# Kernel optimization log

Hardware: AMD Instinct MI355X
Metric: run time of the kernel (lower is better)

The kernel has to match this reference:

```python
import jax, jax.numpy as jnp
import numpy as np

HID = 64      # LSTM hidden size
UH_LEN = 15   # unit-hydrograph length (days)
N_INC = 4     # SAC-SMA sub-steps per day

# (name, lo, hi) -> sigmoid-scaled physical parameter ranges
PARAM_SPECS = [
    ("HAMON_COEF", 0.5, 2.0),
    ("SCF", 0.7, 1.4), ("PXTEMP", -2.0, 2.0), ("MFMAX", 0.5, 2.0), ("MFMIN", 0.05, 0.49),
    ("UADJ", 0.03, 0.19), ("MBASE", 0.0, 1.0), ("TIPM", 0.1, 1.0), ("PLWHC", 0.02, 0.3),
    ("NMF", 0.05, 0.5), ("DAYGM", 0.0, 0.3),
    ("UZTWM", 10.0, 300.0), ("UZFWM", 5.0, 150.0), ("LZTWM", 10.0, 500.0), ("LZFPM", 10.0, 1000.0),
    ("LZFSM", 5.0, 400.0), ("UZK", 0.1, 0.75), ("LZPK", 0.001, 0.05), ("LZSK", 0.01, 0.35),
    ("ZPERC", 5.0, 350.0), ("REXP", 1.0, 5.0), ("PFREE", 0.0, 0.8), ("PCTIM", 0.0, 0.1),
    ("ADIMP", 0.0, 0.4), ("RIVA", 0.0, 0.2), ("SIDE", 0.0, 0.5), ("RSERV", 0.0, 0.4),
    ("THETA_C", 0.0, 1.0), ("UH_N", 1.0, 6.0), ("UH_TAU", 0.5, 5.0),
]


def parameter_net(x_dyn, x_static, Wih, Whh, b_lstm, Ws, bs, Wout, bout):
    """gA: LSTM over dynamic inputs + static encoder -> per-unit physical params."""
    N = x_dyn.shape[0]
    h0 = jnp.zeros((N, HID), x_dyn.dtype)

    def step(carry, xt):
        h, c = carry
        z = xt @ Wih.T + h @ Whh.T + b_lstm
        i, f, g, o = jnp.split(z, 4, axis=-1)
        c = jax.nn.sigmoid(f) * c + jax.nn.sigmoid(i) * jnp.tanh(g)
        h = jax.nn.sigmoid(o) * jnp.tanh(c)
        return (h, c), None

    (h, _), _ = jax.lax.scan(step, (h0, h0), jnp.swapaxes(x_dyn, 0, 1))
    s = jnp.tanh(x_static @ Ws.T + bs)
    raw = jnp.concatenate([h, s], axis=-1) @ Wout.T + bout  # (N, n_params)
    g = jax.nn.sigmoid(raw)
    return {name: lo + g[:, k] * (hi - lo) for k, (name, lo, hi) in enumerate(PARAM_SPECS)}


def hamon_pet(tavg, doyf, lat_rad, coef):
    decl = 0.4093 * jnp.sin(2.0 * jnp.pi / 365.0 * doyf - 1.405)
    cosw = jnp.clip(-jnp.tan(lat_rad[:, None]) * jnp.tan(decl), -0.9999, 0.9999)
    daylen = jnp.arccos(cosw) * 24.0 / jnp.pi                   # hours
    esat = 0.6108 * jnp.exp(17.27 * tavg / (tavg + 237.3))      # kPa
    pet = coef[:, None] * 29.8 * daylen * esat / (tavg + 273.2)
    return jnp.maximum(pet, 0.0)


def run_snow17(prcp, tavg, doyf, elev_m, p):
    SCF, PXTEMP, MFMAX, MFMIN = p['SCF'], p['PXTEMP'], p['MFMAX'], p['MFMIN']
    UADJ, MBASE, TIPM, PLWHC = p['UADJ'], p['MBASE'], p['TIPM'], p['PLWHC']
    NMF, DAYGM = p['NMF'], p['DAYGM']
    pa_fac = jnp.exp(-elev_m / 8434.0)  # atmospheric pressure ratio with elevation

    def step(carry, inp):
        wi, wq, ati = carry
        pr, ta, dy = inp
        is_snow = ta <= PXTEMP
        ps = jnp.where(is_snow, pr * SCF, 0.0)
        prain = jnp.where(is_snow, 0.0, pr)
        wi = wi + ps
        mf = 0.5 * (MFMAX + MFMIN) + 0.5 * (MFMAX - MFMIN) * jnp.sin(2.0 * jnp.pi * dy / 366.0)
        ati = ati + TIPM * (jnp.minimum(ta, 0.0) - ati)
        mros = UADJ * pa_fac * jnp.maximum(ta, 0.0) * jnp.where((~is_snow) & (wi > 0.0), prain, 0.0) * 0.0125
        melt = jnp.clip(mf * jnp.maximum(ta - MBASE, 0.0) + mros - NMF * jnp.maximum(-ati, 0.0), 0.0, wi)
        wi = wi - melt
        gm = jnp.minimum(DAYGM, wi)
        wi = wi - gm
        rain_on_pack = jnp.where(wi > 0.0, prain, 0.0)
        rain_free = prain - rain_on_pack
        wq = wq + melt + rain_on_pack
        out = jnp.maximum(wq - PLWHC * wi, 0.0)
        wq = wq - out
        return (wi, wq, ati), out + gm + rain_free

    z = jnp.zeros_like(p['SCF'])
    _, eff = jax.lax.scan(step, (z, z, z), (prcp.T, tavg.T, doyf.T))
    return eff.T  # (N, T)


def run_sacsma(pav, ep, p, n_inc):
    UZTWM, UZFWM, LZTWM = p['UZTWM'], p['UZFWM'], p['LZTWM']
    LZFPM, LZFSM, UZK = p['LZFPM'], p['LZFSM'], p['UZK']
    LZPK, LZSK, ZPERC, REXP = p['LZPK'], p['LZSK'], p['ZPERC'], p['REXP']
    PFREE, PCTIM, ADIMP, SIDE = p['PFREE'], p['PCTIM'], p['ADIMP'], p['SIDE']
    dt = 1.0 / n_inc
    percm = LZFPM * LZPK + LZFSM * LZSK
    lz_max = LZTWM + LZFPM + LZFSM

    def step(carry, inp):
        uztwc, uzfwc, lztwc, lzfpc, lzfsc, adimc = carry
        pr, e = inp
        # evapotranspiration
        e1 = jnp.minimum(e * uztwc / UZTWM, uztwc); uztwc = uztwc - e1
        red = e - e1
        e2 = jnp.minimum(red, uzfwc); uzfwc = uzfwc - e2; red = red - e2
        e3 = jnp.minimum(red * lztwc / (UZTWM + LZTWM), lztwc); lztwc = lztwc - e3
        # impervious + additional impervious area
        roimp = pr * PCTIM
        padimp = pr * ADIMP
        adimc = adimc + padimp
        adsur = padimp * jnp.clip(adimc / (UZTWM + LZTWM), 0.0, 1.0) ** 2
        adimc = jnp.minimum(adimc - adsur, UZTWM + LZTWM)
        surf = roimp + adsur
        base = jnp.zeros_like(pr)
        pinc = pr * (1.0 - PCTIM - ADIMP) * dt
        for _ in range(n_inc):  # unrolled sub-steps (n_inc is small, static)
            bfp = lzfpc * LZPK * dt; bfs = lzfsc * LZSK * dt
            lzfpc = lzfpc - bfp; lzfsc = lzfsc - bfs
            base = base + (bfp + bfs) / (1.0 + SIDE)
            qif = uzfwc * UZK * dt; uzfwc = uzfwc - qif; surf = surf + qif
            lz_def = (LZTWM - lztwc) + (LZFPM - lzfpc) + (LZFSM - lzfsc)
            defr = jnp.clip(lz_def / lz_max, 1e-6, 1.0)
            perc = percm * (1.0 + ZPERC * defr ** REXP) * dt * uzfwc / UZFWM
            perc = jnp.minimum(jnp.minimum(perc, uzfwc), jnp.maximum(lz_def, 0.0))
            uzfwc = uzfwc - perc
            pfree = perc * PFREE
            lztwc = lztwc + perc - pfree
            ex = jnp.maximum(lztwc - LZTWM, 0.0); lztwc = lztwc - ex; pfree = pfree + ex
            dp = jnp.maximum(LZFPM - lzfpc, 0.0); ds = jnp.maximum(LZFSM - lzfsc, 0.0)
            fr = dp / jnp.maximum(dp + ds, 1e-6)
            lzfpc = lzfpc + pfree * fr; lzfsc = lzfsc + pfree * (1.0 - fr)
            exp_ = jnp.maximum(lzfpc - LZFPM, 0.0); lzfpc = lzfpc - exp_; lzfsc = lzfsc + exp_
            exs = jnp.maximum(lzfsc - LZFSM, 0.0); lzfsc = lzfsc - exs; surf = surf + exs
            uztwc = uztwc + pinc
            exu = jnp.maximum(uztwc - UZTWM, 0.0); uztwc = uztwc - exu
            uzfwc = uzfwc + exu
            exf = jnp.maximum(uzfwc - UZFWM, 0.0); uzfwc = uzfwc - exf
            surf = surf + exf
        return (uztwc, uzfwc, lztwc, lzfpc, lzfsc, adimc), (surf, base)

    init = (0.5 * UZTWM, 0.5 * UZFWM, 0.5 * LZTWM, 0.5 * LZFPM, 0.5 * LZFSM, 0.5 * (UZTWM + LZTWM))
    _, (surf, base) = jax.lax.scan(step, init, (pav.T, ep.T))
    return surf.T, base.T  # (N, T)


def route_lohmann(surf, base, uh_n, uh_tau):
    """Gamma-shaped unit hydrograph per unit; causal convolution over time."""
    t = jnp.arange(1.0, UH_LEN + 1.0)  # (L,)
    w = t[None, :] ** (uh_n[:, None] - 1.0) * jnp.exp(-t[None, :] / uh_tau[:, None])
    uh = w / jnp.sum(w, axis=1, keepdims=True)  # (N, L)
    T = surf.shape[1]
    pad = jnp.pad(surf, ((0, 0), (UH_LEN - 1, 0)))
    q = sum(uh[:, l:l + 1] * pad[:, UH_LEN - 1 - l: UH_LEN - 1 - l + T] for l in range(UH_LEN))
    return q + base


def setup_inputs() -> dict:
    key = jax.random.key(0)
    ks = jax.random.split(key, 13)
    N, T, D_DYN, D_STAT, B = 4000, 730, 8, 16, 200
    NP = len(PARAM_SPECS)
    return {
        'x_dyn': jax.random.normal(ks[0], (N, T, D_DYN), jnp.float32),
        'x_static': jax.random.normal(ks[1], (N, D_STAT), jnp.float32),
        'prcp': 10.0 * jax.random.uniform(ks[2], (N, T), jnp.float32),
        'tavg': 5.0 + 8.0 * jax.random.normal(ks[3], (N, T), jnp.float32),
        'doy': jax.random.randint(ks[4], (N, T), 1, 367, jnp.int32),
        'elev_m': 2500.0 * jax.random.uniform(ks[5], (N,), jnp.float32),
        'lat_rad': 0.2 + 0.6 * jax.random.uniform(ks[6], (N,), jnp.float32),
        'area_weight': jax.random.uniform(ks[7], (N,), jnp.float32),
        'basin_index': jax.random.randint(ks[8], (N,), 0, B, jnp.int32),
        'n_basins': B,
        'Wih': 0.1 * jax.random.normal(ks[9], (4 * HID, D_DYN), jnp.float32),
        'Whh': 0.1 * jax.random.normal(ks[10], (4 * HID, HID), jnp.float32),
        'b_lstm': jnp.zeros((4 * HID,), jnp.float32),
        'Ws': 0.1 * jax.random.normal(ks[11], (HID, D_STAT), jnp.float32),
        'bs': jnp.zeros((HID,), jnp.float32),
        'Wout': 0.1 * jax.random.normal(ks[12], (NP, 2 * HID), jnp.float32),
        'bout': jnp.zeros((NP,), jnp.float32),
    }


def reference(x_dyn, x_static, prcp, tavg, doy, elev_m, lat_rad, area_weight,
              basin_index, n_basins, Wih, Whh, b_lstm, Ws, bs, Wout, bout):
    params = parameter_net(x_dyn, x_static, Wih, Whh, b_lstm, Ws, bs, Wout, bout)
    doyf = doy.astype(jnp.float32)
    pet = hamon_pet(tavg, doyf, lat_rad, params['HAMON_COEF'])
    effective_p = run_snow17(prcp, tavg, doyf, elev_m, params)
    surf, base = run_sacsma(effective_p, pet, params, N_INC)
    q_unit = route_lohmann(surf, base, params['UH_N'], params['UH_TAU'])
    w = area_weight[:, None]
    B = int(n_basins)
    q_gauge = jax.ops.segment_sum(q_unit * w, basin_index, num_segments=B)
    q_base_gauge = jax.ops.segment_sum(base * w, basin_index, num_segments=B)
    return q_gauge, q_base_gauge, q_unit
```

## Files before the change

### kernel.cpp

```cpp
#include <hip/hip_runtime.h>
#include <math.h>

#define HID 64
#define UH_LEN 15
#define N_INC 4

#define TWO_PI_365 0.0172142063f
#define TWO_PI_366 0.0171671554f
#define H24_PI     7.63943727f

typedef short short8 __attribute__((ext_vector_type(8)));
typedef float f32x4  __attribute__((ext_vector_type(4)));

__device__ __forceinline__ float frcp(float x){ return __builtin_amdgcn_rcpf(x); }
__device__ __forceinline__ float sigf(float x){ return frcp(1.0f + __expf(-x)); }
__device__ __forceinline__ float tanhfast(float x){ return 1.0f - 2.0f*frcp(__expf(2.0f*x)+1.0f); }

__device__ __forceinline__ unsigned short f2bf(float f){
    unsigned int u = __float_as_uint(f);
    u += 0x7FFF + ((u >> 16) & 1);
    return (unsigned short)(u >> 16);
}
__device__ __forceinline__ float bf2f(unsigned short h){
    return __uint_as_float(((unsigned int)h) << 16);
}

__device__ const float PLO[30] = {0.5f,0.7f,-2.0f,0.5f,0.05f,0.03f,0.0f,0.1f,0.02f,0.05f,0.0f,
                                  10.0f,5.0f,10.0f,10.0f,5.0f,0.1f,0.001f,0.01f,5.0f,1.0f,0.0f,
                                  0.0f,0.0f,0.0f,0.0f,0.0f,0.0f,1.0f,0.5f};
__device__ const float PHI[30] = {2.0f,1.4f,2.0f,2.0f,0.49f,0.19f,1.0f,1.0f,0.3f,0.5f,0.3f,
                                  300.0f,150.0f,500.0f,1000.0f,400.0f,0.75f,0.05f,0.35f,350.0f,5.0f,0.8f,
                                  0.1f,0.4f,0.2f,0.5f,0.4f,1.0f,6.0f,5.0f};
__device__ const float LOGT[15] = {0.0f,0.69314718f,1.09861229f,1.38629436f,1.60943791f,
                                   1.79175947f,1.94591015f,2.07944154f,2.19722458f,2.30258509f,
                                   2.39789527f,2.48490665f,2.56494936f,2.63905733f,2.70805020f};

__global__ void zero_kernel(float* __restrict__ p, int cnt){
    int i = blockIdx.x*256 + threadIdx.x;
    if (i < cnt) p[i] = 0.0f;
}

__global__ __launch_bounds__(256) void xpack_kernel(
    const float* __restrict__ x_dyn, unsigned short* __restrict__ xb, size_t NT)
{
    size_t i = (size_t)blockIdx.x*256 + threadIdx.x;
    if (i >= NT) return;
    const float4 a = ((const float4*)x_dyn)[2*i];
    const float4 b = ((const float4*)x_dyn)[2*i + 1];
    short8 o;
    o[0]=(short)f2bf(a.x); o[1]=(short)f2bf(a.y); o[2]=(short)f2bf(a.z); o[3]=(short)f2bf(a.w);
    o[4]=(short)f2bf(b.x); o[5]=(short)f2bf(b.y); o[6]=(short)f2bf(b.z); o[7]=(short)f2bf(b.w);
    ((short8*)xb)[i] = o;
}

template<bool XB>
__global__ __launch_bounds__(256, 2) void lstm_kernel(
    const float* __restrict__ x_dyn, const unsigned short* __restrict__ xb,
    const float* __restrict__ x_static,
    const float* __restrict__ Wih, const float* __restrict__ Whh,
    const float* __restrict__ b_lstm, const float* __restrict__ Ws,
    const float* __restrict__ bs, const float* __restrict__ Wout,
    const float* __restrict__ bout, float* __restrict__ params,
    int N, int T, int DSTAT)
{
    __shared__ unsigned short h_lds[2][16*64];
    __shared__ float s_sh[16*64];

    const int tid = threadIdx.x;
    const int wv  = tid >> 6;
    const int ln  = tid & 63;
    const int q   = ln >> 4;
    const int r16 = ln & 15;
    const int u0  = blockIdx.x * 8;

    short8 wf[4][3];
    float  bias[4];
    #pragma unroll
    for (int g = 0; g < 4; ++g) {
        const int n = 64*g + 16*wv + r16;
        bias[g] = b_lstm[n];
        #pragma unroll
        for (int kb = 0; kb < 3; ++kb) {
            short8 w;
            #pragma unroll
            for (int e = 0; e < 8; ++e) {
                int k = 32*kb + 8*q + e;
                float v = 0.0f;
                if (k < 64)      v = Whh[n*64 + k];
                else if (k < 72) v = Wih[n*8 + (k - 64)];
                w[e] = (short)f2bf(v);
            }
            wf[g][kb] = w;
        }
    }

    for (int i = tid; i < 2*16*64; i += 256) ((unsigned short*)h_lds)[i] = 0;
    __syncthreads();

    float c[4] = {0.f, 0.f, 0.f, 0.f};

    const int ux = min(u0 + r16, N-1);
    short8 xcur;
    #pragma unroll
    for (int e = 0; e < 8; ++e) xcur[e] = 0;
    short8 xnxt = xcur;
    float xf[8];
    if (q == 0) {
        if (XB) {
            xcur = *(const short8*)(xb + ((size_t)ux*T)*8);
            xnxt = xcur;
        } else {
            const float* p = x_dyn + ((size_t)ux * T) * 8;
            #pragma unroll
            for (int e = 0; e < 8; ++e) xf[e] = p[e];
        }
    }

    const int jj   = 16*wv + r16;
    const int swz0 = (q       ^ (r16 & 7)) << 3;
    const int swz1 = ((q + 4) ^ (r16 & 7)) << 3;

    for (int t = 0; t < T; ++t) {
        short8 a2;
        if (XB) {
            a2 = xcur;
        } else {
            #pragma unroll
            for (int e = 0; e < 8; ++e) a2[e] = (q == 0) ? (short)f2bf(xf[e]) : (short)0;
        }

        const int rb = t & 1;
        short8 a0 = *(const short8*)&h_lds[rb][r16*64 + swz0];
        short8 a1 = *(const short8*)&h_lds[rb][r16*64 + swz1];

        if (q == 0) {
            const int tn = min(t + 1, T - 1);
            if (XB) {
                xnxt = *(const short8*)(xb + ((size_t)ux*T + tn)*8);
            } else if (t + 1 < T) {
                const float* p = x_dyn + ((size_t)ux * T + (t+1)) * 8;
                #pragma unroll
                for (int e = 0; e < 8; ++e) xf[e] = p[e];
            }
        }

        f32x4 acc[4];
        #pragma unroll
        for (int g = 0; g < 4; ++g) {
            f32x4 a; a[0]=bias[g]; a[1]=bias[g]; a[2]=bias[g]; a[3]=bias[g];
            a = __builtin_amdgcn_mfma_f32_16x16x32_bf16(a2, wf[g][2], a, 0, 0, 0);
            a = __builtin_amdgcn_mfma_f32_16x16x32_bf16(a0, wf[g][0], a, 0, 0, 0);
            a = __builtin_amdgcn_mfma_f32_16x16x32_bf16(a1, wf[g][1], a, 0, 0, 0);
            acc[g] = a;
        }

        const int wb = rb ^ 1;
        #pragma unroll
        for (int r = 0; r < 4; ++r) {
            float iv = sigf(acc[0][r]);
            float fv = sigf(acc[1][r]);
            float gv = tanhfast(acc[2][r]);
            float ov = sigf(acc[3][r]);
            c[r] = fv*c[r] + iv*gv;
            float hv = ov*tanhfast(c[r]);
            int u = 4*q + r;
            h_lds[wb][u*64 + (((jj>>3) ^ (u&7))<<3) + (jj&7)] = f2bf(hv);
        }
        if (XB) xcur = xnxt;
        __syncthreads();
    }

    const int fb = T & 1;
    for (int uu = 0; uu < 4; ++uu) {
        int ul = wv*4 + uu;
        int u  = min(u0 + ul, N-1);
        float a = bs[ln];
        for (int k = 0; k < DSTAT; ++k)
            a = fmaf(x_static[(size_t)u*DSTAT + k], Ws[ln*DSTAT + k], a);
        s_sh[ul*64 + ln] = tanhfast(a);
    }
    if (ln < 30) {
        for (int uu = 0; uu < 4; ++uu) {
            int ul = wv*4 + uu;
            int unit = u0 + ul;
            if (unit < N) {
                float raw = bout[ln];
                #pragma unroll 8
                for (int m = 0; m < 64; ++m) {
                    float hm = bf2f(h_lds[fb][ul*64 + (((m>>3) ^ (ul&7))<<3) + (m&7)]);
                    float sm = s_sh[ul*64 + m];
                    raw = fmaf(hm, Wout[ln*128 + m],      raw);
                    raw = fmaf(sm, Wout[ln*128 + 64 + m], raw);
                }
                float g = sigf(raw);
                params[ln*N + unit] = PLO[ln] + g*(PHI[ln] - PLO[ln]);
            }
        }
    }
}

__global__ __launch_bounds__(256) void pack_kernel(
    const float* __restrict__ prcp, const float* __restrict__ tavg,
    const int* __restrict__ doy, const float* __restrict__ lat_rad,
    const float* __restrict__ P,
    float4* __restrict__ pack, int N, int T)
{
    const int n = blockIdx.y;
    const int t = blockIdx.x*256 + threadIdx.x;
    if (t >= T) return;
    const float pr = prcp[(size_t)n*T + t];
    const float ta = tavg[(size_t)n*T + t];
    const float dy = (float)doy[(size_t)n*T + t];
    const float tanlat = __tanf(lat_rad[n]);
    const float HAMON  = P[n];
    const float MFMAX  = P[3*N + n], MFMIN = P[4*N + n];
    float decl  = 0.4093f*__sinf(TWO_PI_365*dy - 1.405f);
    float cosw  = fminf(fmaxf(-tanlat*__tanf(decl), -0.9999f), 0.9999f);
    float daylen= acosf(cosw)*H24_PI;
    float esat  = 0.6108f*__expf(17.27f*ta*frcp(ta + 237.3f));
    float pet   = fmaxf(HAMON*29.8f*daylen*esat*frcp(ta + 273.2f), 0.0f);
    float mf    = 0.5f*(MFMAX + MFMIN) + 0.5f*(MFMAX - MFMIN)*__sinf(TWO_PI_366*dy);
    pack[(size_t)n*T + t] = make_float4(pr, ta, pet, mf);
}

template<bool PACKED, bool SPLIT>
__global__ __launch_bounds__(64, 1) void physics_kernel(
    const float* __restrict__ prcp, const float* __restrict__ tavg,
    const int*   __restrict__ doy,  const float* __restrict__ elev_m,
    const float* __restrict__ lat_rad, const float* __restrict__ area_w,
    const int*   __restrict__ basin_idx, const float* __restrict__ P,
    const float4* __restrict__ pack, float2* __restrict__ sbA,
    float* __restrict__ surfA, float* __restrict__ baseA,
    float* __restrict__ out, int N, int T, int B)
{
    int n = blockIdx.x*64 + threadIdx.x;
    if (n >= N) return;

    const float HAMON = P[ 0*N+n], SCF   = P[ 1*N+n], PXTEMP= P[ 2*N+n];
    const float MFMAX = P[ 3*N+n], MFMIN = P[ 4*N+n];
    const float MBASE = P[ 6*N+n], TIPM  = P[ 7*N+n], PLWHC = P[ 8*N+n];
    const float NMF   = P[ 9*N+n], DAYGM = P[10*N+n];
    const float UZTWM = P[11*N+n], UZFWM = P[12*N+n], LZTWM = P[13*N+n];
    const float LZFPM = P[14*N+n], LZFSM = P[15*N+n], UZK   = P[16*N+n];
    const float LZPK  = P[17*N+n], LZSK  = P[18*N+n], ZPERC = P[19*N+n];
    const float REXP  = P[20*N+n], PFREE = P[21*N+n], PCTIM = P[22*N+n];
    const float ADIMP = P[23*N+n], SIDE  = P[25*N+n];
    const float UH_N  = P[28*N+n], UH_TAU= P[29*N+n];

    const float mrosk  = P[5*N+n]*__expf(-elev_m[n]*(1.0f/8434.0f))*0.0125f;
    const float tanlat = __tanf(lat_rad[n]);
    const float wA     = area_w[n];
    const int   bi     = basin_idx[n];
    const float mfa = 0.5f*(MFMAX + MFMIN), mfb = 0.5f*(MFMAX - MFMIN);

    float uh[UH_LEN];
    float hist[UH_LEN-1];
    if (!SPLIT) {
        float uhs = 0.0f;
        const float inv_tau = frcp(UH_TAU);
        #pragma unroll
        for (int l = 0; l < UH_LEN; ++l) {
            uh[l] = __expf((UH_N - 1.0f)*LOGT[l] - (float)(l+1)*inv_tau);
            uhs += uh[l];
        }
        float inv_uhs = frcp(uhs);
        #pragma unroll
        for (int l = 0; l < UH_LEN; ++l) uh[l] *= inv_uhs;
        #pragma unroll
        for (int l = 0; l < UH_LEN-1; ++l) hist[l] = 0.0f;
    }

    const float dtq       = 1.0f / (float)N_INC;
    const float kp        = LZPK*dtq, ks = LZSK*dtq, ku = UZK*dtq;
    const float twm_sum   = UZTWM + LZTWM;
    const float inv_uztwm = frcp(UZTWM);
    const float inv_twm   = frcp(twm_sum);
    const float inv_lzmax = frcp(LZTWM + LZFPM + LZFSM);
    const float inv_side  = frcp(1.0f + SIDE);
    const float pinc_fac  = (1.0f - PCTIM - ADIMP)*dtq;
    const float pm        = (LZFPM*LZPK + LZFSM*LZSK)*dtq*frcp(UZFWM);

    float wi = 0.0f, wq = 0.0f, ati = 0.0f;
    float uztwc = 0.5f*UZTWM, uzfwc = 0.5f*UZFWM, lztwc = 0.5f*LZTWM;
    float lzfpc = 0.5f*LZFPM, lzfsc = 0.5f*LZFSM, adimc = 0.5f*twm_sum;

    float* q_gauge = out;
    float* q_base  = out + (size_t)B*T;
    float* q_unit  = out + (size_t)2*B*T;

    const float4* pk = PACKED ? (pack + (size_t)n*T) : nullptr;
    float2*       sb = PACKED ? (sbA  + (size_t)n*T) : nullptr;
    float4 cur, nx1;
    float pr_c, ta_c, pet_c, mf_c;
    if (PACKED) {
        cur = pk[0];
        nx1 = pk[T > 1 ? 1 : 0];
    } else {
        pr_c = prcp[(size_t)n*T];
        ta_c = tavg[(size_t)n*T];
        float dy = (float)doy[(size_t)n*T];
        float decl = 0.4093f*__sinf(TWO_PI_365*dy - 1.405f);
        float cosw = fminf(fmaxf(-tanlat*__tanf(decl), -0.9999f), 0.9999f);
        pet_c = fmaxf(HAMON*29.8f*(acosf(cosw)*H24_PI)
                      *0.6108f*__expf(17.27f*ta_c*frcp(ta_c + 237.3f))
                      *frcp(ta_c + 273.2f), 0.0f);
        mf_c  = mfa + mfb*__sinf(TWO_PI_366*dy);
    }

    for (int t = 0; t < T; ++t) {
        float pr, ta, pet, mf;
        float4 nx2;
        float pr_n, ta_n, dy_n;
        if (PACKED) {
            nx2 = pk[min(t + 2, T - 1)];
            pr = cur.x; ta = cur.y; pet = cur.z; mf = cur.w;
        } else {
            const int tn = min(t + 1, T - 1);
            pr_n = prcp[(size_t)n*T + tn];
            ta_n = tavg[(size_t)n*T + tn];
            dy_n = (float)doy[(size_t)n*T + tn];
            pr = pr_c; ta = ta_c; pet = pet_c; mf = mf_c;
        }

        bool is_snow = (ta <= PXTEMP);
        float ps    = is_snow ? pr*SCF : 0.0f;
        float prain = is_snow ? 0.0f   : pr;
        wi += ps;
        ati += TIPM*(fminf(ta, 0.0f) - ati);
        float mros = mrosk*fmaxf(ta, 0.0f)*((!is_snow && wi > 0.0f) ? prain : 0.0f);
        float melt = fminf(fmaxf(mf*fmaxf(ta - MBASE, 0.0f) + mros - NMF*fmaxf(-ati, 0.0f), 0.0f), wi);
        wi -= melt;
        float gm = fminf(DAYGM, wi);
        wi -= gm;
        float rop   = (wi > 0.0f) ? prain : 0.0f;
        float rfree = prain - rop;
        wq += melt + rop;
        float outq = fmaxf(wq - PLWHC*wi, 0.0f);
        wq -= outq;
        float eff = outq + gm + rfree;

        float e1 = fminf(pet*uztwc*inv_uztwm, uztwc);
        uztwc -= e1;
        float red = pet - e1;
        float e2 = fminf(red, uzfwc);
        uzfwc -= e2; red -= e2;
        float e3 = fminf(red*lztwc*inv_twm, lztwc);
        lztwc -= e3;
        float roimp  = eff*PCTIM;
        float padimp = eff*ADIMP;
        adimc += padimp;
        float ratio = fminf(fmaxf(adimc*inv_twm, 0.0f), 1.0f);
        float adsur = padimp*ratio*ratio;
        adimc = fminf(adimc - adsur, twm_sum);
        float surf = roimp + adsur;
        float base = 0.0f;
// ... 1 lines not shown
        #pragma unroll
        for (int inc = 0; inc < N_INC; ++inc) {
            float bfp = lzfpc*kp;
            float bfs = lzfsc*ks;
            lzfpc -= bfp; lzfsc -= bfs;
            base += (bfp + bfs)*inv_side;
            float qif = uzfwc*ku;
            uzfwc -= qif; surf += qif;
            float lz_def = (LZTWM - lztwc) + (LZFPM - lzfpc) + (LZFSM - lzfsc);
            float defr = fminf(fmaxf(lz_def*inv_lzmax, 1e-6f), 1.0f);
            float perc = pm*fmaf(ZPERC, __expf(REXP*__logf(defr)), 1.0f)*uzfwc;
            perc = fminf(fminf(perc, uzfwc), fmaxf(lz_def, 0.0f));
            uzfwc -= perc;
            float pfree = perc*PFREE;
            lztwc += perc - pfree;
            float ex = fmaxf(lztwc - LZTWM, 0.0f);
            lztwc -= ex; pfree += ex;
            float dp  = fmaxf(LZFPM - lzfpc, 0.0f);
            float dsx = fmaxf(LZFSM - lzfsc, 0.0f);
            float fr  = dp*frcp(fmaxf(dp + dsx, 1e-6f));
            lzfpc += pfree*fr;
            lzfsc += pfree*(1.0f - fr);
            float exq = fmaxf(lzfpc - LZFPM, 0.0f);
            lzfpc -= exq; lzfsc += exq;
            float exs = fmaxf(lzfsc - LZFSM, 0.0f);
            lzfsc -= exs; surf += exs;
            uztwc += pinc;
            float exu = fmaxf(uztwc - UZTWM, 0.0f);
            uztwc -= exu; uzfwc += exu;
            float exf = fmaxf(uzfwc - UZFWM, 0.0f);
            uzfwc -= exf; surf += exf;
        }

        if (PACKED) {
            sb[t] = make_float2(surf, base);
            cur = nx1; nx1 = nx2;
        } else if (SPLIT) {
            surfA[(size_t)n*T + t] = surf;
            baseA[(size_t)n*T + t] = base;
        } else {
            float qv = uh[0]*surf;
            #pragma unroll
            for (int l = 1; l < UH_LEN; ++l) qv = fmaf(uh[l], hist[l-1], qv);
            #pragma unroll
            for (int l = UH_LEN-2; l >= 1; --l) hist[l] = hist[l-1];
            hist[0] = surf;
            qv += base;
            q_unit[(size_t)n*T + t] = qv;
            atomicAdd(&q_gauge[(size_t)bi*T + t], qv*wA);
            atomicAdd(&q_base [(size_t)bi*T + t], base*wA);
        }

        if (!PACKED) {
            float decl = 0.4093f*__sinf(TWO_PI_365*dy_n - 1.405f);
            float cosw = fminf(fmaxf(-tanlat*__tanf(decl), -0.9999f), 0.9999f);
            pet_c = fmaxf(HAMON*29.8f*(acosf(cosw)*H24_PI)
                          *0.6108f*__expf(17.27f*ta_n*frcp(ta_n + 237.3f))
                          *frcp(ta_n + 273.2f), 0.0f);
            mf_c = mfa + mfb*__sinf(TWO_PI_366*dy_n);
            pr_c = pr_n; ta_c = ta_n;
        }
    }
}

template<bool PACKED>
__global__ __launch_bounds__(256) void route_kernel(
    const float2* __restrict__ sbA,
    const float* __restrict__ surfA, const float* __restrict__ baseA,
    const float* __restrict__ P, const float* __restrict__ area_w,
    const int* __restrict__ basin_idx,
    float* __restrict__ out, int N, int T, int B)
{
    __shared__ float uh_sh[UH_LEN];
    __shared__ float wA_sh;
    __shared__ int   bi_sh;

    const int n = blockIdx.y;
    const int t = blockIdx.x*256 + threadIdx.x;

    if (threadIdx.x == 0) {
        float UH_N = P[28*N + n], UH_TAU = P[29*N + n];
        float inv_tau = frcp(UH_TAU);
        float tmp[UH_LEN], s = 0.f;
        #pragma unroll
        for (int l = 0; l < UH_LEN; ++l) {
            tmp[l] = __expf((UH_N - 1.0f)*LOGT[l] - (float)(l+1)*inv_tau);
            s += tmp[l];
        }
        float is = frcp(s);
        #pragma unroll
        for (int l = 0; l < UH_LEN; ++l) uh_sh[l] = tmp[l]*is;
        wA_sh = area_w[n];
        bi_sh = basin_idx[n];
    }
// ... 48 lines not shown
    const float* Ws       = (const float*)d_in[13];
    const float* bs       = (const float*)d_in[14];
    const float* Wout     = (const float*)d_in[15];
    const float* bout     = (const float*)d_in[16];

    const int N = in_sizes[7];
    const int T = in_sizes[2] / N;
    const int DSTAT = in_sizes[1] / N;
    const size_t NT = (size_t)N * T;
    const int B = (out_size - (int)NT) / (2 * T);

    char* wsb = (char*)d_ws;
    float* params = (float*)wsb;
    const size_t off_prm = align256(30*(size_t)N*sizeof(float));

    const size_t off_xb0   = off_prm;
    const size_t off_pack0 = align256(off_xb0 + NT*16);
    const size_t off_sb0   = align256(off_pack0 + NT*16);
    const size_t need0     = off_sb0 + NT*8;
    const size_t off_pack1 = off_prm;
    const size_t off_sb1   = align256(off_pack1 + NT*16);
    const size_t need1     = off_sb1 + NT*8;
    const size_t off_surf2 = off_prm;
    const size_t off_base2 = off_surf2 + NT*4;
    const size_t need2     = off_base2 + NT*4;

    const int tier = (ws_size >= need0) ? 0 : (ws_size >= need1) ? 1 :
                     (ws_size >= need2) ? 2 : 3;

    float* out = (float*)d_out;
    const int zc = 2 * B * T;
    zero_kernel<<<(zc + 255)/256, 256, 0, stream>>>(out, zc);

    const int blocks_lstm = (N + 7) / 8;
    const int pblocks = (N + 63) / 64;
    dim3 rg((T + 255)/256, N);

    if (tier == 0) {
        unsigned short* xbp = (unsigned short*)(wsb + off_xb0);
        float4* pack = (float4*)(wsb + off_pack0);
        float2* sbA  = (float2*)(wsb + off_sb0);
        xpack_kernel<<<(int)((NT + 255)/256), 256, 0, stream>>>(x_dyn, xbp, NT);
        lstm_kernel<true><<<blocks_lstm, 256, 0, stream>>>(
            x_dyn, xbp, x_static, Wih, Whh, b_lstm, Ws, bs, Wout, bout,
            params, N, T, DSTAT);
        pack_kernel<<<rg, 256, 0, stream>>>(prcp, tavg, doy, lat_rad, params, pack, N, T);
        physics_kernel<true, true><<<pblocks, 64, 0, stream>>>(
            prcp, tavg, doy, elev_m, lat_rad, area_w, basin_ix, params,
            pack, sbA, nullptr, nullptr, out, N, T, B);
        route_kernel<true><<<rg, 256, 0, stream>>>(sbA, nullptr, nullptr, params, area_w,
                                                   basin_ix, out, N, T, B);
    } else if (tier == 1) {
        float4* pack = (float4*)(wsb + off_pack1);
        float2* sbA  = (float2*)(wsb + off_sb1);
        lstm_kernel<false><<<blocks_lstm, 256, 0, stream>>>(
            x_dyn, nullptr, x_static, Wih, Whh, b_lstm, Ws, bs, Wout, bout,
            params, N, T, DSTAT);
        pack_kernel<<<rg, 256, 0, stream>>>(prcp, tavg, doy, lat_rad, params, pack, N, T);
        physics_kernel<true, true><<<pblocks, 64, 0, stream>>>(
            prcp, tavg, doy, elev_m, lat_rad, area_w, basin_ix, params,
            pack, sbA, nullptr, nullptr, out, N, T, B);
        route_kernel<true><<<rg, 256, 0, stream>>>(sbA, nullptr, nullptr, params, area_w,
                                                   basin_ix, out, N, T, B);
    } else if (tier == 2) {
        float* surfA = (float*)(wsb + off_surf2);
        float* baseA = (float*)(wsb + off_base2);
        lstm_kernel<false><<<blocks_lstm, 256, 0, stream>>>(
            x_dyn, nullptr, x_static, Wih, Whh, b_lstm, Ws, bs, Wout, bout,
            params, N, T, DSTAT);
        physics_kernel<false, true><<<pblocks, 64, 0, stream>>>(
            prcp, tavg, doy, elev_m, lat_rad, area_w, basin_ix, params,
            nullptr, nullptr, surfA, baseA, out, N, T, B);
        route_kernel<false><<<rg, 256, 0, stream>>>(nullptr, surfA, baseA, params, area_w,
                                                    basin_ix, out, N, T, B);
    } else {
        lstm_kernel<false><<<blocks_lstm, 256, 0, stream>>>(
            x_dyn, nullptr, x_static, Wih, Whh, b_lstm, Ws, bs, Wout, bout,
            params, N, T, DSTAT);
        physics_kernel<false, false><<<pblocks, 64, 0, stream>>>(
            prcp, tavg, doy, elev_m, lat_rad, area_w, basin_ix, params,
            nullptr, nullptr, nullptr, nullptr, out, N, T, B);
    }
}
```

Before: 1.262 ms.

## Remove duplicate LSTM units per block and process two units per physics thread

The LSTM block stride goes from 8 to 16 units, so each 16-row MFMA tile covers distinct units instead of overlapping the next block. This halves the LSTM block count, and the launch bound drops to one block per CU. The bf16-input time loop is unrolled by two with explicit LDS waits and raw barriers, and the x loads are prefetched two steps ahead. A new physics2 kernel runs Snow-17 and SAC-SMA for two units per thread to interleave two independent serial recurrences for more ILP, at the cost of half as many threads and higher register pressure.

```diff
diff --git a/kernel.cpp b/kernel.cpp
--- a/kernel.cpp
+++ b/kernel.cpp
@@ -54,7 +54,7 @@
 }
 
 template<bool XB>
-__global__ __launch_bounds__(256, 2) void lstm_kernel(
+__global__ __launch_bounds__(256, 1) void lstm_kernel(
     const float* __restrict__ x_dyn, const unsigned short* __restrict__ xb,
     const float* __restrict__ x_static,
     const float* __restrict__ Wih, const float* __restrict__ Whh,
@@ -71,7 +71,7 @@
     const int ln  = tid & 63;
     const int q   = ln >> 4;
     const int r16 = ln & 15;
-    const int u0  = blockIdx.x * 8;
+    const int u0  = blockIdx.x * 16;
 
     short8 wf[4][3];
     float  bias[4];
@@ -100,75 +100,99 @@
     float c[4] = {0.f, 0.f, 0.f, 0.f};
 
     const int ux = min(u0 + r16, N-1);
-    short8 xcur;
-    #pragma unroll
-    for (int e = 0; e < 8; ++e) xcur[e] = 0;
-    short8 xnxt = xcur;
-    float xf[8];
-    if (q == 0) {
-        if (XB) {
-            xcur = *(const short8*)(xb + ((size_t)ux*T)*8);
-            xnxt = xcur;
-        } else {
+    const int jj   = 16*wv + r16;
+    const int swz0 = (q       ^ (r16 & 7)) << 3;
+    const int swz1 = ((q + 4) ^ (r16 & 7)) << 3;
+
+#define LSTM_STEP(T_CUR, RB, XREG)                                              \
+    {                                                                           \
+        short8 a0 = *(const short8*)&h_lds[RB][r16*64 + swz0];                  \
+        short8 a1 = *(const short8*)&h_lds[RB][r16*64 + swz1];                  \
+        short8 a2 = XREG;                                                       \
+        if (q == 0)                                                             \
+            XREG = *(const short8*)(xb + ((size_t)ux*T + min((T_CUR)+2, T-1))*8);\
+        f32x4 acc[4];                                                           \
+        _Pragma("unroll")                                                       \
+        for (int gg = 0; gg < 4; ++gg) {                                        \
+            f32x4 a; a[0]=bias[gg]; a[1]=bias[gg]; a[2]=bias[gg]; a[3]=bias[gg];\
+            a = __builtin_amdgcn_mfma_f32_16x16x32_bf16(a2, wf[gg][2], a,0,0,0);\
+            a = __builtin_amdgcn_mfma_f32_16x16x32_bf16(a0, wf[gg][0], a,0,0,0);\
+            a = __builtin_amdgcn_mfma_f32_16x16x32_bf16(a1, wf[gg][1], a,0,0,0);\
+            acc[gg] = a;                                                        \
+        }                                                                       \
+        _Pragma("unroll")                                                       \
+        for (int r = 0; r < 4; ++r) {                                           \
+            float iv = sigf(acc[0][r]);                                         \
+            float fv = sigf(acc[1][r]);                                         \
+            float gv = tanhfast(acc[2][r]);                                     \
+            float ov = sigf(acc[3][r]);                                         \
+            c[r] = fv*c[r] + iv*gv;                                             \
+            float hv = ov*tanhfast(c[r]);                                       \
+            int u = 4*q + r;                                                    \
+            h_lds[(RB)^1][u*64 + (((jj>>3) ^ (u&7))<<3) + (jj&7)] = f2bf(hv);   \
+        }                                                                       \
+        asm volatile("s_waitcnt lgkmcnt(0)" ::: "memory");                      \
+        __builtin_amdgcn_s_barrier();                                           \
+    }
+
+    if constexpr (XB) {
+        short8 x0, x1;
+        #pragma unroll
+        for (int e = 0; e < 8; ++e) { x0[e] = 0; x1[e] = 0; }
+        if (q == 0) {
+            x0 = *(const short8*)(xb + ((size_t)ux*T)*8);
+            x1 = *(const short8*)(xb + ((size_t)ux*T + min(1, T-1))*8);
+        }
+        int t = 0;
+        for (; t + 1 < T; t += 2) {
+            LSTM_STEP(t,   0, x0);
+            LSTM_STEP(t+1, 1, x1);
+        }
+        if (t < T) LSTM_STEP(t, 0, x0);
+    } else {
+        float xf[8];
+        if (q == 0) {
             const float* p = x_dyn + ((size_t)ux * T) * 8;
             #pragma unroll
             for (int e = 0; e < 8; ++e) xf[e] = p[e];
         }
-    }
-
-    const int jj   = 16*wv + r16;
-    const int swz0 = (q       ^ (r16 & 7)) << 3;
-    const int swz1 = ((q + 4) ^ (r16 & 7)) << 3;
-
-    for (int t = 0; t < T; ++t) {
-        short8 a2;
-        if (XB) {
-            a2 = xcur;
-        } else {
+        for (int t = 0; t < T; ++t) {
+            short8 a2;
             #pragma unroll
             for (int e = 0; e < 8; ++e) a2[e] = (q == 0) ? (short)f2bf(xf[e]) : (short)0;
-        }
-
-        const int rb = t & 1;
-        short8 a0 = *(const short8*)&h_lds[rb][r16*64 + swz0];
-        short8 a1 = *(const short8*)&h_lds[rb][r16*64 + swz1];
-
-        if (q == 0) {
-            const int tn = min(t + 1, T - 1);
-            if (XB) {
-                xnxt = *(const short8*)(xb + ((size_t)ux*T + tn)*8);
-            } else if (t + 1 < T) {
+            const int rb = t & 1;
+            short8 a0 = *(const short8*)&h_lds[rb][r16*64 + swz0];
+            short8 a1 = *(const short8*)&h_lds[rb][r16*64 + swz1];
+            if (q == 0 && t + 1 < T) {
                 const float* p = x_dyn + ((size_t)ux * T + (t+1)) * 8;
                 #pragma unroll
                 for (int e = 0; e < 8; ++e) xf[e] = p[e];
             }
-        }
-
-        f32x4 acc[4];
-        #pragma unroll
-        for (int g = 0; g < 4; ++g) {
-            f32x4 a; a[0]=bias[g]; a[1]=bias[g]; a[2]=bias[g]; a[3]=bias[g];
-            a = __builtin_amdgcn_mfma_f32_16x16x32_bf16(a2, wf[g][2], a, 0, 0, 0);
-            a = __builtin_amdgcn_mfma_f32_16x16x32_bf16(a0, wf[g][0], a, 0, 0, 0);
-            a = __builtin_amdgcn_mfma_f32_16x16x32_bf16(a1, wf[g][1], a, 0, 0, 0);
-            acc[g] = a;
-        }
-
-        const int wb = rb ^ 1;
-        #pragma unroll
-        for (int r = 0; r < 4; ++r) {
-            float iv = sigf(acc[0][r]);
-            float fv = sigf(acc[1][r]);
-            float gv = tanhfast(acc[2][r]);
-            float ov = sigf(acc[3][r]);
-            c[r] = fv*c[r] + iv*gv;
-            float hv = ov*tanhfast(c[r]);
-            int u = 4*q + r;
-            h_lds[wb][u*64 + (((jj>>3) ^ (u&7))<<3) + (jj&7)] = f2bf(hv);
-        }
-        if (XB) xcur = xnxt;
-        __syncthreads();
-    }
+            f32x4 acc[4];
+            #pragma unroll
+            for (int g = 0; g < 4; ++g) {
+                f32x4 a; a[0]=bias[g]; a[1]=bias[g]; a[2]=bias[g]; a[3]=bias[g];
+                a = __builtin_amdgcn_mfma_f32_16x16x32_bf16(a2, wf[g][2], a, 0, 0, 0);
+                a = __builtin_amdgcn_mfma_f32_16x16x32_bf16(a0, wf[g][0], a, 0, 0, 0);
+                a = __builtin_amdgcn_mfma_f32_16x16x32_bf16(a1, wf[g][1], a, 0, 0, 0);
+                acc[g] = a;
+            }
+            const int wb = rb ^ 1;
+            #pragma unroll
+            for (int r = 0; r < 4; ++r) {
+                float iv = sigf(acc[0][r]);
+                float fv = sigf(acc[1][r]);
+                float gv = tanhfast(acc[2][r]);
+                float ov = sigf(acc[3][r]);
+                c[r] = fv*c[r] + iv*gv;
+                float hv = ov*tanhfast(c[r]);
+                int u = 4*q + r;
+                h_lds[wb][u*64 + (((jj>>3) ^ (u&7))<<3) + (jj&7)] = f2bf(hv);
+            }
+            __syncthreads();
+        }
+    }
+#undef LSTM_STEP
 
     const int fb = T & 1;
     for (int uu = 0; uu < 4; ++uu) {
@@ -223,13 +247,152 @@
     pack[(size_t)n*T + t] = make_float4(pr, ta, pet, mf);
 }
 
-template<bool PACKED, bool SPLIT>
+__global__ __launch_bounds__(64, 1) void physics2_kernel(
+    const float* __restrict__ elev_m, const float* __restrict__ P,
+    const float4* __restrict__ pack, float2* __restrict__ sbA, int N, int T)
+{
+    const int g  = blockIdx.x*64 + threadIdx.x;
+    const int n0 = 2*g;
+    if (n0 >= N) return;
+    int nn[2]; nn[0] = n0; nn[1] = min(n0 + 1, N - 1);
+
+    float SCF[2],PXTEMP[2],MBASE[2],TIPM[2],PLWHC[2],NMF[2],DAYGM[2];
+    float UZTWM[2],UZFWM[2],LZTWM[2],LZFPM[2],LZFSM[2];
+    float mrosk[2],iUZTWM[2],itwm[2],twm[2],ilzmax[2],iside[2],pfac[2];
+    float kp[2],ks[2],ku[2],pm[2],ZPERC[2],REXP[2],PFREE[2],PCTIM[2],ADIMP[2];
+    const float dtq = 1.0f / (float)N_INC;
+    #pragma unroll
+    for (int u = 0; u < 2; ++u) {
+        const int n = nn[u];
+        SCF[u]=P[1*N+n]; PXTEMP[u]=P[2*N+n];
+        mrosk[u]=P[5*N+n]*__expf(-elev_m[n]*(1.0f/8434.0f))*0.0125f;
+        MBASE[u]=P[6*N+n]; TIPM[u]=P[7*N+n]; PLWHC[u]=P[8*N+n];
+        NMF[u]=P[9*N+n]; DAYGM[u]=P[10*N+n];
+        UZTWM[u]=P[11*N+n]; UZFWM[u]=P[12*N+n]; LZTWM[u]=P[13*N+n];
+        LZFPM[u]=P[14*N+n]; LZFSM[u]=P[15*N+n];
+        ku[u]=P[16*N+n]*dtq;
+        float LZPK=P[17*N+n], LZSK=P[18*N+n];
+        kp[u]=LZPK*dtq; ks[u]=LZSK*dtq;
+        pm[u]=(LZFPM[u]*LZPK + LZFSM[u]*LZSK)*dtq*frcp(UZFWM[u]);
+        ZPERC[u]=P[19*N+n]; REXP[u]=P[20*N+n]; PFREE[u]=P[21*N+n];
+        PCTIM[u]=P[22*N+n]; ADIMP[u]=P[23*N+n];
+        iside[u]=frcp(1.0f + P[25*N+n]);
+        pfac[u]=(1.0f - PCTIM[u] - ADIMP[u])*dtq;
+        iUZTWM[u]=frcp(UZTWM[u]);
+        twm[u]=UZTWM[u]+LZTWM[u]; itwm[u]=frcp(twm[u]);
+        ilzmax[u]=frcp(LZTWM[u]+LZFPM[u]+LZFSM[u]);
+    }
+
+    float wi[2]={0.f,0.f}, wqv[2]={0.f,0.f}, ati[2]={0.f,0.f};
+    float uztwc[2],uzfwc[2],lztwc[2],lzfpc[2],lzfsc[2],adimc[2];
+    #pragma unroll
+    for (int u = 0; u < 2; ++u) {
+        uztwc[u]=0.5f*UZTWM[u]; uzfwc[u]=0.5f*UZFWM[u]; lztwc[u]=0.5f*LZTWM[u];
+        lzfpc[u]=0.5f*LZFPM[u]; lzfsc[u]=0.5f*LZFSM[u]; adimc[u]=0.5f*twm[u];
+    }
+
+    const float4* pk0 = pack + (size_t)nn[0]*T;
+    const float4* pk1 = pack + (size_t)nn[1]*T;
+    float2* sb0 = sbA + (size_t)nn[0]*T;
+    float2* sb1 = sbA + (size_t)nn[1]*T;
+
+    float4 cur[2], nx1[2];
+    cur[0] = pk0[0]; cur[1] = pk1[0];
+    const int t1i = min(1, T-1);
+    nx1[0] = pk0[t1i]; nx1[1] = pk1[t1i];
+
+    for (int t = 0; t < T; ++t) {
+        const int t2 = min(t + 2, T - 1);
+        float4 nx2_0 = pk0[t2];
+        float4 nx2_1 = pk1[t2];
+
+        float sfo[2], bso[2];
+        #pragma unroll
+        for (int u = 0; u < 2; ++u) {
+            const float pr = cur[u].x, ta = cur[u].y, pet = cur[u].z, mf = cur[u].w;
+
+            bool is_snow = (ta <= PXTEMP[u]);
+            float ps    = is_snow ? pr*SCF[u] : 0.0f;
+            float prain = is_snow ? 0.0f : pr;
+            wi[u] += ps;
+            ati[u] += TIPM[u]*(fminf(ta, 0.0f) - ati[u]);
+            float mros = mrosk[u]*fmaxf(ta, 0.0f)*((!is_snow && wi[u] > 0.0f) ? prain : 0.0f);
+            float melt = fminf(fmaxf(mf*fmaxf(ta - MBASE[u], 0.0f) + mros
+                                     - NMF[u]*fmaxf(-ati[u], 0.0f), 0.0f), wi[u]);
+            wi[u] -= melt;
+            float gm = fminf(DAYGM[u], wi[u]);
+            wi[u] -= gm;
+            float rop   = (wi[u] > 0.0f) ? prain : 0.0f;
+            float rfree = prain - rop;
+            wqv[u] += melt + rop;
+            float outq = fmaxf(wqv[u] - PLWHC[u]*wi[u], 0.0f);
+            wqv[u] -= outq;
+            float eff = outq + gm + rfree;
+
+            float e1 = fminf(pet*uztwc[u]*iUZTWM[u], uztwc[u]);
+            uztwc[u] -= e1;
+            float red = pet - e1;
+            float e2 = fminf(red, uzfwc[u]);
+            uzfwc[u] -= e2; red -= e2;
+            float e3 = fminf(red*lztwc[u]*itwm[u], lztwc[u]);
+            lztwc[u] -= e3;
+            float roimp  = eff*PCTIM[u];
+            float padimp = eff*ADIMP[u];
+            adimc[u] += padimp;
+            float ratio = fminf(fmaxf(adimc[u]*itwm[u], 0.0f), 1.0f);
+            float adsur = padimp*ratio*ratio;
+            adimc[u] = fminf(adimc[u] - adsur, twm[u]);
+            float surf = roimp + adsur;
+            float base = 0.0f;
+            float pinc = eff*pfac[u];
+            #pragma unroll
+            for (int inc = 0; inc < N_INC; ++inc) {
+                float bfp = lzfpc[u]*kp[u];
+                float bfs = lzfsc[u]*ks[u];
+                lzfpc[u] -= bfp; lzfsc[u] -= bfs;
+                base += (bfp + bfs)*iside[u];
+                float qif = uzfwc[u]*ku[u];
+                uzfwc[u] -= qif; surf += qif;
+                float lz_def = (LZTWM[u]-lztwc[u]) + (LZFPM[u]-lzfpc[u]) + (LZFSM[u]-lzfsc[u]);
+                float defr = fminf(fmaxf(lz_def*ilzmax[u], 1e-6f), 1.0f);
+                float perc = pm[u]*fmaf(ZPERC[u], __expf(REXP[u]*__logf(defr)), 1.0f)*uzfwc[u];
+                perc = fminf(fminf(perc, uzfwc[u]), fmaxf(lz_def, 0.0f));
+                uzfwc[u] -= perc;
+                float pfree = perc*PFREE[u];
+                lztwc[u] += perc - pfree;
+                float ex = fmaxf(lztwc[u] - LZTWM[u], 0.0f);
+                lztwc[u] -= ex; pfree += ex;
+                float dp  = fmaxf(LZFPM[u] - lzfpc[u], 0.0f);
+                float dsx = fmaxf(LZFSM[u] - lzfsc[u], 0.0f);
+                float fr  = dp*frcp(fmaxf(dp + dsx, 1e-6f));
+                lzfpc[u] += pfree*fr;
+                lzfsc[u] += pfree*(1.0f - fr);
+                float exq = fmaxf(lzfpc[u] - LZFPM[u], 0.0f);
+                lzfpc[u] -= exq; lzfsc[u] += exq;
+                float exs = fmaxf(lzfsc[u] - LZFSM[u], 0.0f);
+                lzfsc[u] -= exs; surf += exs;
+                uztwc[u] += pinc;
+                float exu = fmaxf(uztwc[u] - UZTWM[u], 0.0f);
+                uztwc[u] -= exu; uzfwc[u] += exu;
+                float exf = fmaxf(uzfwc[u] - UZFWM[u], 0.0f);
+                uzfwc[u] -= exf; surf += exf;
+            }
+            sfo[u] = surf; bso[u] = base;
+        }
+
+        sb0[t] = make_float2(sfo[0], bso[0]);
+        sb1[t] = make_float2(sfo[1], bso[1]);
+        cur[0] = nx1[0]; cur[1] = nx1[1];
+        nx1[0] = nx2_0;  nx1[1] = nx2_1;
+    }
+}
+
+template<bool SPLIT>
 __global__ __launch_bounds__(64, 1) void physics_kernel(
     const float* __restrict__ prcp, const float* __restrict__ tavg,
     const int*   __restrict__ doy,  const float* __restrict__ elev_m,
     const float* __restrict__ lat_rad, const float* __restrict__ area_w,
     const int*   __restrict__ basin_idx, const float* __restrict__ P,
-    const float4* __restrict__ pack, float2* __restrict__ sbA,
     float* __restrict__ surfA, float* __restrict__ baseA,
     float* __restrict__ out, int N, int T, int B)
 {
@@ -288,39 +451,22 @@
     float* q_base  = out + (size_t)B*T;
     float* q_unit  = out + (size_t)2*B*T;
 
-    const float4* pk = PACKED ? (pack + (size_t)n*T) : nullptr;
-    float2*       sb = PACKED ? (sbA  + (size_t)n*T) : nullptr;
-    float4 cur, nx1;
-    float pr_c, ta_c, pet_c, mf_c;
-    if (PACKED) {
-        cur = pk[0];
-        nx1 = pk[T > 1 ? 1 : 0];
-    } else {
-        pr_c = prcp[(size_t)n*T];
-        ta_c = tavg[(size_t)n*T];
-        float dy = (float)doy[(size_t)n*T];
-        float decl = 0.4093f*__sinf(TWO_PI_365*dy - 1.405f);
-        float cosw = fminf(fmaxf(-tanlat*__tanf(decl), -0.9999f), 0.9999f);
-        pet_c = fmaxf(HAMON*29.8f*(acosf(cosw)*H24_PI)
-                      *0.6108f*__expf(17.27f*ta_c*frcp(ta_c + 237.3f))
-                      *frcp(ta_c + 273.2f), 0.0f);
-        mf_c  = mfa + mfb*__sinf(TWO_PI_366*dy);
-    }
+    float pr_c = prcp[(size_t)n*T];
+    float ta_c = tavg[(size_t)n*T];
+    float dy0 = (float)doy[(size_t)n*T];
+    float decl0 = 0.4093f*__sinf(TWO_PI_365*dy0 - 1.405f);
+    float cosw0 = fminf(fmaxf(-tanlat*__tanf(decl0), -0.9999f), 0.9999f);
+    float pet_c = fmaxf(HAMON*29.8f*(acosf(cosw0)*H24_PI)
+                        *0.6108f*__expf(17.27f*ta_c*frcp(ta_c + 237.3f))
+                        *frcp(ta_c + 273.2f), 0.0f);
+    float mf_c  = mfa + mfb*__sinf(TWO_PI_366*dy0);
 
     for (int t = 0; t < T; ++t) {
-        float pr, ta, pet, mf;
-        float4 nx2;
-        float pr_n, ta_n, dy_n;
-        if (PACKED) {
-            nx2 = pk[min(t + 2, T - 1)];
-            pr = cur.x; ta = cur.y; pet = cur.z; mf = cur.w;
-        } else {
-            const int tn = min(t + 1, T - 1);
-            pr_n = prcp[(size_t)n*T + tn];
-            ta_n = tavg[(size_t)n*T + tn];
-            dy_n = (float)doy[(size_t)n*T + tn];
-            pr = pr_c; ta = ta_c; pet = pet_c; mf = mf_c;
-        }
+        const int tn = min(t + 1, T - 1);
+        float pr_n = prcp[(size_t)n*T + tn];
+        float ta_n = tavg[(size_t)n*T + tn];
+        float dy_n = (float)doy[(size_t)n*T + tn];
+        const float pr = pr_c, ta = ta_c, pet = pet_c, mf = mf_c;
 
         bool is_snow = (ta <= PXTEMP);
         float ps    = is_snow ? pr*SCF : 0.0f;
@@ -388,10 +534,7 @@
             uzfwc -= exf; surf += exf;
         }
 
-        if (PACKED) {
-            sb[t] = make_float2(surf, base);
-            cur = nx1; nx1 = nx2;
-        } else if (SPLIT) {
+        if (SPLIT) {
             surfA[(size_t)n*T + t] = surf;
             baseA[(size_t)n*T + t] = base;
         } else {
@@ -407,15 +550,13 @@
             atomicAdd(&q_base [(size_t)bi*T + t], base*wA);
         }
 
-        if (!PACKED) {
-            float decl = 0.4093f*__sinf(TWO_PI_365*dy_n - 1.405f);
-            float cosw = fminf(fmaxf(-tanlat*__tanf(decl), -0.9999f), 0.9999f);
-            pet_c = fmaxf(HAMON*29.8f*(acosf(cosw)*H24_PI)
-                          *0.6108f*__expf(17.27f*ta_n*frcp(ta_n + 237.3f))
-                          *frcp(ta_n + 273.2f), 0.0f);
-            mf_c = mfa + mfb*__sinf(TWO_PI_366*dy_n);
-            pr_c = pr_n; ta_c = ta_n;
-        }
+        float decl = 0.4093f*__sinf(TWO_PI_365*dy_n - 1.405f);
+        float cosw = fminf(fmaxf(-tanlat*__tanf(decl), -0.9999f), 0.9999f);
+        pet_c = fmaxf(HAMON*29.8f*(acosf(cosw)*H24_PI)
+                      *0.6108f*__expf(17.27f*ta_n*frcp(ta_n + 237.3f))
+                      *frcp(ta_n + 273.2f), 0.0f);
+        mf_c = mfa + mfb*__sinf(TWO_PI_366*dy_n);
+        pr_c = pr_n; ta_c = ta_n;
     }
 }
 
@@ -530,7 +671,9 @@
     const int zc = 2 * B * T;
     zero_kernel<<<(zc + 255)/256, 256, 0, stream>>>(out, zc);
 
-    const int blocks_lstm = (N + 7) / 8;
+    const int blocks_lstm = (N + 15) / 16;
+    const int npairs = (N + 1) / 2;
+    const int p2blocks = (npairs + 63) / 64;
     const int pblocks = (N + 63) / 64;
     dim3 rg((T + 255)/256, N);
 
@@ -543,9 +686,7 @@
             x_dyn, xbp, x_static, Wih, Whh, b_lstm, Ws, bs, Wout, bout,
             params, N, T, DSTAT);
         pack_kernel<<<rg, 256, 0, stream>>>(prcp, tavg, doy, lat_rad, params, pack, N, T);
-        physics_kernel<true, true><<<pblocks, 64, 0, stream>>>(
-            prcp, tavg, doy, elev_m, lat_rad, area_w, basin_ix, params,
-            pack, sbA, nullptr, nullptr, out, N, T, B);
+        physics2_kernel<<<p2blocks, 64, 0, stream>>>(elev_m, params, pack, sbA, N, T);
         route_kernel<true><<<rg, 256, 0, stream>>>(sbA, nullptr, nullptr, params, area_w,
                                                    basin_ix, out, N, T, B);
     } else if (tier == 1) {
@@ -555,9 +696,7 @@
             x_dyn, nullptr, x_static, Wih, Whh, b_lstm, Ws, bs, Wout, bout,
             params, N, T, DSTAT);
         pack_kernel<<<rg, 256, 0, stream>>>(prcp, tavg, doy, lat_rad, params, pack, N, T);
-        physics_kernel<true, true><<<pblocks, 64, 0, stream>>>(
-            prcp, tavg, doy, elev_m, lat_rad, area_w, basin_ix, params,
-            pack, sbA, nullptr, nullptr, out, N, T, B);
+        physics2_kernel<<<p2blocks, 64, 0, stream>>>(elev_m, params, pack, sbA, N, T);
         route_kernel<true><<<rg, 256, 0, stream>>>(sbA, nullptr, nullptr, params, area_w,
                                                    basin_ix, out, N, T, B);
     } else if (tier == 2) {
@@ -566,17 +705,17 @@
         lstm_kernel<false><<<blocks_lstm, 256, 0, stream>>>(
             x_dyn, nullptr, x_static, Wih, Whh, b_lstm, Ws, bs, Wout, bout,
             params, N, T, DSTAT);
-        physics_kernel<false, true><<<pblocks, 64, 0, stream>>>(
+        physics_kernel<true><<<pblocks, 64, 0, stream>>>(
             prcp, tavg, doy, elev_m, lat_rad, area_w, basin_ix, params,
-            nullptr, nullptr, surfA, baseA, out, N, T, B);
+            surfA, baseA, out, N, T, B);
         route_kernel<false><<<rg, 256, 0, stream>>>(nullptr, surfA, baseA, params, area_w,
                                                     basin_ix, out, N, T, B);
     } else {
         lstm_kernel<false><<<blocks_lstm, 256, 0, stream>>>(
             x_dyn, nullptr, x_static, Wih, Whh, b_lstm, Ws, bs, Wout, bout,
             params, N, T, DSTAT);
-        physics_kernel<false, false><<<pblocks, 64, 0, stream>>>(
+        physics_kernel<false><<<pblocks, 64, 0, stream>>>(
             prcp, tavg, doy, elev_m, lat_rad, area_w, basin_ix, params,
-            nullptr, nullptr, nullptr, nullptr, out, N, T, B);
-    }
-}
+            nullptr, nullptr, out, N, T, B);
+    }
+}
```

Result: slower. 1.642 ms (+30.0%).

## Map 16 units per LSTM block and unroll recurrence with prefetched inputs

Applied to the files above, without the earlier changes.

Each LSTM block now owns 16 units, matching the 16-row MFMA tile, instead of 8. The old overlapping tiling made neighbouring blocks recompute the same rows, so this halves the block count and that redundant recurrent work. The XB time loop is also unrolled by two, keeps two input registers prefetched two steps ahead, and replaces __syncthreads with an explicit lgkmcnt wait plus s_barrier. Launch bounds are relaxed to one block per SM, which trades occupancy for register headroom.

```diff
diff --git a/kernel.cpp b/kernel.cpp
--- a/kernel.cpp
+++ b/kernel.cpp
@@ -54,7 +54,7 @@
 }
 
 template<bool XB>
-__global__ __launch_bounds__(256, 2) void lstm_kernel(
+__global__ __launch_bounds__(256, 1) void lstm_kernel(
     const float* __restrict__ x_dyn, const unsigned short* __restrict__ xb,
     const float* __restrict__ x_static,
     const float* __restrict__ Wih, const float* __restrict__ Whh,
@@ -71,7 +71,7 @@
     const int ln  = tid & 63;
     const int q   = ln >> 4;
     const int r16 = ln & 15;
-    const int u0  = blockIdx.x * 8;
+    const int u0  = blockIdx.x * 16;
 
     short8 wf[4][3];
     float  bias[4];
@@ -100,75 +100,99 @@
     float c[4] = {0.f, 0.f, 0.f, 0.f};
 
     const int ux = min(u0 + r16, N-1);
-    short8 xcur;
-    #pragma unroll
-    for (int e = 0; e < 8; ++e) xcur[e] = 0;
-    short8 xnxt = xcur;
-    float xf[8];
-    if (q == 0) {
-        if (XB) {
-            xcur = *(const short8*)(xb + ((size_t)ux*T)*8);
-            xnxt = xcur;
-        } else {
+    const int jj   = 16*wv + r16;
+    const int swz0 = (q       ^ (r16 & 7)) << 3;
+    const int swz1 = ((q + 4) ^ (r16 & 7)) << 3;
+
+#define LSTM_STEP(T_CUR, RB, XREG)                                              \
+    {                                                                           \
+        short8 a0 = *(const short8*)&h_lds[RB][r16*64 + swz0];                  \
+        short8 a1 = *(const short8*)&h_lds[RB][r16*64 + swz1];                  \
+        short8 a2 = XREG;                                                       \
+        if (q == 0)                                                             \
+            XREG = *(const short8*)(xb + ((size_t)ux*T + min((T_CUR)+2, T-1))*8);\
+        f32x4 acc[4];                                                           \
+        _Pragma("unroll")                                                       \
+        for (int gg = 0; gg < 4; ++gg) {                                        \
+            f32x4 a; a[0]=bias[gg]; a[1]=bias[gg]; a[2]=bias[gg]; a[3]=bias[gg];\
+            a = __builtin_amdgcn_mfma_f32_16x16x32_bf16(a2, wf[gg][2], a,0,0,0);\
+            a = __builtin_amdgcn_mfma_f32_16x16x32_bf16(a0, wf[gg][0], a,0,0,0);\
+            a = __builtin_amdgcn_mfma_f32_16x16x32_bf16(a1, wf[gg][1], a,0,0,0);\
+            acc[gg] = a;                                                        \
+        }                                                                       \
+        _Pragma("unroll")                                                       \
+        for (int r = 0; r < 4; ++r) {                                           \
+            float iv = sigf(acc[0][r]);                                         \
+            float fv = sigf(acc[1][r]);                                         \
+            float gv = tanhfast(acc[2][r]);                                     \
+            float ov = sigf(acc[3][r]);                                         \
+            c[r] = fv*c[r] + iv*gv;                                             \
+            float hv = ov*tanhfast(c[r]);                                       \
+            int u = 4*q + r;                                                    \
+            h_lds[(RB)^1][u*64 + (((jj>>3) ^ (u&7))<<3) + (jj&7)] = f2bf(hv);   \
+        }                                                                       \
+        asm volatile("s_waitcnt lgkmcnt(0)" ::: "memory");                      \
+        __builtin_amdgcn_s_barrier();                                           \
+    }
+
+    if constexpr (XB) {
+        short8 x0, x1;
+        #pragma unroll
+        for (int e = 0; e < 8; ++e) { x0[e] = 0; x1[e] = 0; }
+        if (q == 0) {
+            x0 = *(const short8*)(xb + ((size_t)ux*T)*8);
+            x1 = *(const short8*)(xb + ((size_t)ux*T + min(1, T-1))*8);
+        }
+        int t = 0;
+        for (; t + 1 < T; t += 2) {
+            LSTM_STEP(t,   0, x0);
+            LSTM_STEP(t+1, 1, x1);
+        }
+        if (t < T) LSTM_STEP(t, 0, x0);
+    } else {
+        float xf[8];
+        if (q == 0) {
             const float* p = x_dyn + ((size_t)ux * T) * 8;
             #pragma unroll
             for (int e = 0; e < 8; ++e) xf[e] = p[e];
         }
-    }
-
-    const int jj   = 16*wv + r16;
-    const int swz0 = (q       ^ (r16 & 7)) << 3;
-    const int swz1 = ((q + 4) ^ (r16 & 7)) << 3;
-
-    for (int t = 0; t < T; ++t) {
-        short8 a2;
-        if (XB) {
-            a2 = xcur;
-        } else {
+        for (int t = 0; t < T; ++t) {
+            short8 a2;
             #pragma unroll
             for (int e = 0; e < 8; ++e) a2[e] = (q == 0) ? (short)f2bf(xf[e]) : (short)0;
-        }
-
-        const int rb = t & 1;
-        short8 a0 = *(const short8*)&h_lds[rb][r16*64 + swz0];
-        short8 a1 = *(const short8*)&h_lds[rb][r16*64 + swz1];
-
-        if (q == 0) {
-            const int tn = min(t + 1, T - 1);
-            if (XB) {
-                xnxt = *(const short8*)(xb + ((size_t)ux*T + tn)*8);
-            } else if (t + 1 < T) {
+            const int rb = t & 1;
+            short8 a0 = *(const short8*)&h_lds[rb][r16*64 + swz0];
+            short8 a1 = *(const short8*)&h_lds[rb][r16*64 + swz1];
+            if (q == 0 && t + 1 < T) {
                 const float* p = x_dyn + ((size_t)ux * T + (t+1)) * 8;
                 #pragma unroll
                 for (int e = 0; e < 8; ++e) xf[e] = p[e];
             }
-        }
-
-        f32x4 acc[4];
-        #pragma unroll
-        for (int g = 0; g < 4; ++g) {
-            f32x4 a; a[0]=bias[g]; a[1]=bias[g]; a[2]=bias[g]; a[3]=bias[g];
-            a = __builtin_amdgcn_mfma_f32_16x16x32_bf16(a2, wf[g][2], a, 0, 0, 0);
-            a = __builtin_amdgcn_mfma_f32_16x16x32_bf16(a0, wf[g][0], a, 0, 0, 0);
-            a = __builtin_amdgcn_mfma_f32_16x16x32_bf16(a1, wf[g][1], a, 0, 0, 0);
-            acc[g] = a;
-        }
-
-        const int wb = rb ^ 1;
-        #pragma unroll
-        for (int r = 0; r < 4; ++r) {
-            float iv = sigf(acc[0][r]);
-            float fv = sigf(acc[1][r]);
-            float gv = tanhfast(acc[2][r]);
-            float ov = sigf(acc[3][r]);
-            c[r] = fv*c[r] + iv*gv;
-            float hv = ov*tanhfast(c[r]);
-            int u = 4*q + r;
-            h_lds[wb][u*64 + (((jj>>3) ^ (u&7))<<3) + (jj&7)] = f2bf(hv);
-        }
-        if (XB) xcur = xnxt;
-        __syncthreads();
-    }
+            f32x4 acc[4];
+            #pragma unroll
+            for (int g = 0; g < 4; ++g) {
+                f32x4 a; a[0]=bias[g]; a[1]=bias[g]; a[2]=bias[g]; a[3]=bias[g];
+                a = __builtin_amdgcn_mfma_f32_16x16x32_bf16(a2, wf[g][2], a, 0, 0, 0);
+                a = __builtin_amdgcn_mfma_f32_16x16x32_bf16(a0, wf[g][0], a, 0, 0, 0);
+                a = __builtin_amdgcn_mfma_f32_16x16x32_bf16(a1, wf[g][1], a, 0, 0, 0);
+                acc[g] = a;
+            }
+            const int wb = rb ^ 1;
+            #pragma unroll
+            for (int r = 0; r < 4; ++r) {
+                float iv = sigf(acc[0][r]);
+                float fv = sigf(acc[1][r]);
+                float gv = tanhfast(acc[2][r]);
+                float ov = sigf(acc[3][r]);
+                c[r] = fv*c[r] + iv*gv;
+                float hv = ov*tanhfast(c[r]);
+                int u = 4*q + r;
+                h_lds[wb][u*64 + (((jj>>3) ^ (u&7))<<3) + (jj&7)] = f2bf(hv);
+            }
+            __syncthreads();
+        }
+    }
+#undef LSTM_STEP
 
     const int fb = T & 1;
     for (int uu = 0; uu < 4; ++uu) {
@@ -530,7 +554,7 @@
     const int zc = 2 * B * T;
     zero_kernel<<<(zc + 255)/256, 256, 0, stream>>>(out, zc);
 
-    const int blocks_lstm = (N + 7) / 8;
+    const int blocks_lstm = (N + 15) / 16;
     const int pblocks = (N + 63) / 64;
     dim3 rg((T + 255)/256, N);
 
```

New measurement: 1.064 ms. -15.7%, faster.
